# Performance work log

Measured on AMD Instinct MI355X. Metric: run time of the kernel, lower is better.

The kernel has to match this reference:

```python
import jax, jax.numpy as jnp
import numpy as np

PH, PW = 7, 7
ALPHA = 0.5


def setup_inputs() -> dict:
    key = jax.random.key(0)
    k1, k2 = jax.random.split(key)
    x = jax.random.normal(k1, (4, 128, 224, 224), dtype=jnp.float32)
    beta = jax.random.normal(k2, (1,), dtype=jnp.float32)
    return {"x": x, "beta": beta}


def reference(x, beta):
    B, C, H, W = x.shape
    Hh, Ww = H // PH, W // PW
    M = Hh * Ww
    P = PH * PW
    # non-overlapping unfold: (B,C,H,W) -> (B*M, C, P), patches row-major over (Hh,Ww),
    # pixel order within patch is row-major (i*PW+j), matching F.unfold
    flat = (
        x.reshape(B, C, Hh, PH, Ww, PW)
        .transpose(0, 2, 4, 1, 3, 5)  # (B,Hh,Ww,C,PH,PW)
        .reshape(B * M, C, P)
    )
    # channel-similarity attention: (BM,C,C)
    Sc_big = jax.nn.softmax(jnp.einsum("ncp,ndp->ncd", flat, flat), axis=-1)
    # channel covariance: (BM,C,C)
    d = flat - flat.mean(axis=-1, keepdims=True)
    cov_C = jnp.einsum("ncp,ndp->ncd", d, d) / P
    # only the top-left CxC block of L_big is ever used downstream
    # (Mc_big, cov_S and the padded S-block are dead computation in the original)
    Ec_big = jnp.einsum("ncd,ndp->ncp", Sc_big + ALPHA * cov_C, flat)  # (BM,C,P)
    # fold back (inverse of the non-overlapping unfold)
    Ec_map = (
        Ec_big.reshape(B, Hh, Ww, C, PH, PW)
        .transpose(0, 3, 1, 4, 2, 5)  # (B,C,Hh,PH,Ww,PW)
        .reshape(B, C, H, W)
    )
    attention_map = beta[0] * Ec_map + x
    out = x * attention_map
    return (out, Sc_big.reshape(B, M, C, C), cov_C.reshape(B, M, C, C), Ec_map)
```

## Files before the change

kernel.cpp:

```cpp
#include <hip/hip_runtime.h>


#define CCH 128
#define SF_STR 60
#define SA_STR 136

typedef __attribute__((ext_vector_type(8))) unsigned short ushort8v;

static __device__ __forceinline__ unsigned short f2bf(float f) {
    unsigned u = __builtin_bit_cast(unsigned, f);
    u = (u + 0x7FFFu + ((u >> 16) & 1u)) >> 16;
    return (unsigned short)u;
}
static __device__ __forceinline__ float bf2f(unsigned short h) {
    return __builtin_bit_cast(float, ((unsigned)h) << 16);
}

__global__ __launch_bounds__(512, 4)
void bdca_kernel(const float* __restrict__ x, const float* __restrict__ betap,
                 float* __restrict__ out, float* __restrict__ sc_out,
                 float* __restrict__ cov_out, float* __restrict__ ec_out)
{
    __shared__ float sF[CCH * SF_STR];
    __shared__ unsigned short sA[CCH * SA_STR];

    const int bm = blockIdx.x;
    const int b  = bm >> 10;
    const int hh = (bm >> 5) & 31;
    const int ww = bm & 31;
    const int t  = threadIdx.x;
    const float beta = betap[0];

    const float* xpatch = x + (size_t)b * (CCH * 50176) + (hh * 7) * 224 + (ww * 7);

    for (int r = t; r < CCH * 7; r += 512) {
        int c = r / 7, i = r - c * 7;
        const float* src = xpatch + (size_t)c * 50176 + i * 224;
        float* dst = &sF[c * SF_STR + i * 8];
        #pragma unroll
        for (int j = 0; j < 7; ++j) dst[j] = src[j];
    }
    __syncthreads();

    if (t < CCH) {
        const float* row = &sF[t * SF_STR];
        float s = 0.f;
        #pragma unroll
        for (int sl = 0; sl < 7; ++sl) {
            #pragma unroll
            for (int k = 0; k < 7; ++k) s += row[sl * 8 + k];
        }
        sF[t * SF_STR + 56] = s * (1.f / 49.f);
    }
    __syncthreads();

    const int rg = t >> 4;
    const int cg = t & 15;
    float g[4][8];
    #pragma unroll
    for (int i = 0; i < 4; ++i)
        #pragma unroll
        for (int j = 0; j < 8; ++j) g[i][j] = 0.f;

    #pragma unroll 1
    for (int sl = 0; sl < 7; ++sl) {
        float av[4][7];
        #pragma unroll
        for (int i = 0; i < 4; ++i) {
            const float* ap = &sF[(rg + 32 * i) * SF_STR + sl * 8];
            float4 a4 = *(const float4*)ap;
            float2 a2 = *(const float2*)(ap + 4);
            float  a6 = ap[6];
            av[i][0] = a4.x; av[i][1] = a4.y; av[i][2] = a4.z; av[i][3] = a4.w;
            av[i][4] = a2.x; av[i][5] = a2.y; av[i][6] = a6;
        }
        #pragma unroll
        for (int j = 0; j < 8; ++j) {
            const float* bp = &sF[(cg + 16 * j) * SF_STR + sl * 8];
            float4 b4 = *(const float4*)bp;
            float2 b2 = *(const float2*)(bp + 4);
            float  b6 = bp[6];
            float bv[7] = {b4.x, b4.y, b4.z, b4.w, b2.x, b2.y, b6};
            #pragma unroll
            for (int i = 0; i < 4; ++i)
                #pragma unroll
                for (int k = 0; k < 7; ++k)
                    g[i][j] = fmaf(av[i][k], bv[k], g[i][j]);
        }
    }

    const size_t scbase = (size_t)bm * (CCH * CCH);
    float mud[8];
    #pragma unroll
    for (int j = 0; j < 8; ++j) mud[j] = sF[(cg + 16 * j) * SF_STR + 56];

    #pragma unroll
    for (int i = 0; i < 4; ++i) {
        const int c = rg + 32 * i;
        float m = g[i][0];
        #pragma unroll
        for (int j = 1; j < 8; ++j) m = fmaxf(m, g[i][j]);
        #pragma unroll
        for (int msk = 1; msk <= 8; msk <<= 1) m = fmaxf(m, __shfl_xor(m, msk, 64));
        float e[8];
        float s = 0.f;
        #pragma unroll
        for (int j = 0; j < 8; ++j) { e[j] = __expf(g[i][j] - m); s += e[j]; }
        #pragma unroll
        for (int msk = 1; msk <= 8; msk <<= 1) s += __shfl_xor(s, msk, 64);
        const float rinv = 1.f / s;
        const float muc  = sF[c * SF_STR + 56];
        const size_t rowb = scbase + (size_t)c * CCH;
        #pragma unroll
        for (int j = 0; j < 8; ++j) {
            const int d = cg + 16 * j;
            const float sc = e[j] * rinv;
            const float cv = g[i][j] * (1.f / 49.f) - muc * mud[j];
            sc_out[rowb + d]  = sc;
            cov_out[rowb + d] = cv;
            sA[c * SA_STR + d] = f2bf(fmaf(0.5f, cv, sc));
        }
    }
    __syncthreads();

    if (t < 448) {
        const int dq  = t & 3;
        const int cg2 = (t >> 2) & 15;
        const int pg  = t >> 6;
        float acc[8][7];
        #pragma unroll
        for (int i = 0; i < 8; ++i)
            #pragma unroll
            for (int k = 0; k < 7; ++k) acc[i][k] = 0.f;

        #pragma unroll 1
        for (int jc = 0; jc < 4; ++jc) {
            const int d0 = dq * 32 + jc * 8;
            ushort8v av[8];
            #pragma unroll
            for (int i = 0; i < 8; ++i)
                av[i] = *(const ushort8v*)&sA[(cg2 + 16 * i) * SA_STR + d0];
            #pragma unroll
            for (int q = 0; q < 8; ++q) {
                const float* fp = &sF[(d0 + q) * SF_STR + pg * 8];
                float4 f4 = *(const float4*)fp;
                float2 f2 = *(const float2*)(fp + 4);
                float  f6 = fp[6];
                float fv[7] = {f4.x, f4.y, f4.z, f4.w, f2.x, f2.y, f6};
                #pragma unroll
                for (int i = 0; i < 8; ++i) {
                    const float aval = bf2f(av[i][q]);
                    #pragma unroll
                    for (int k = 0; k < 7; ++k)
                        acc[i][k] = fmaf(aval, fv[k], acc[i][k]);
                }
            }
        }
        #pragma unroll
        for (int i = 0; i < 8; ++i) {
            #pragma unroll
            for (int k = 0; k < 7; ++k) {
                float v = acc[i][k];
                v += __shfl_xor(v, 1, 64);
                v += __shfl_xor(v, 2, 64);
                acc[i][k] = v;
            }
        }

        #pragma unroll
        for (int i = 0; i < 8; ++i) {
            if ((i >> 1) == dq) {
                const int c = cg2 + 16 * i;
                const float* xrow = &sF[c * SF_STR + pg * 8];
                const size_t gaddr =
                    ((size_t)(b * CCH + c) * 224 + (hh * 7 + pg)) * 224 + (ww * 7);
                #pragma unroll
                for (int k = 0; k < 7; ++k) {
                    const float ec = acc[i][k];
                    const float xv = xrow[k];
                    ec_out[gaddr + k] = ec;
                    out[gaddr + k]    = xv * fmaf(beta, ec, xv);
                }
            }
        }
    }
}

extern "C" void kernel_launch(void* const* d_in, const int* in_sizes, int n_in,
                              void* d_out, int out_size, void* d_ws, size_t ws_size,
                              hipStream_t stream)
{
    const float* x    = (const float*)d_in[0];
    const float* beta = (const float*)d_in[1];
    float* out = (float*)d_out;
    float* sc  = out + 25690112;
    float* cov = sc  + 67108864;
    float* ec  = cov + 67108864;
    bdca_kernel<<<dim3(4096), dim3(512), 0, stream>>>(x, beta, out, sc, cov, ec);
}
```

Before: 1.108 ms.

## Swizzle patch smem layout, remap block order, use nontemporal stores for sc/cov

Changes the shared-memory patch buffer to a 64-float row stride with an XOR swizzle on 4-float chunks, so the vector loads in both GEMM phases avoid bank conflicts. Remaps block indices so consecutive workgroups come from different regions of the patch grid, which changes the global access pattern and L2/channel spread. Writes the large Sc and cov outputs with nontemporal stores so this streaming write traffic does not pollute the caches. The swizzle adds index arithmetic and splits each row access into two chunk addresses.

```diff
diff --git a/kernel.cpp b/kernel.cpp
--- a/kernel.cpp
+++ b/kernel.cpp
@@ -2,7 +2,7 @@
 
 
 #define CCH 128
-#define SF_STR 60
+#define SF_STR 64
 #define SA_STR 136
 
 typedef __attribute__((ext_vector_type(8))) unsigned short ushort8v;
@@ -14,6 +14,9 @@
 }
 static __device__ __forceinline__ float bf2f(unsigned short h) {
     return __builtin_bit_cast(float, ((unsigned)h) << 16);
+}
+static __device__ __forceinline__ int sfx(int row, int col) {
+    return (row << 6) + (col ^ (((row ^ (row >> 5)) & 7) << 2));
 }
 
 __global__ __launch_bounds__(512, 4)
@@ -24,7 +27,8 @@
     __shared__ float sF[CCH * SF_STR];
     __shared__ unsigned short sA[CCH * SA_STR];
 
-    const int bm = blockIdx.x;
+    const int bid = blockIdx.x;
+    const int bm  = (bid & 7) * 512 + (bid >> 3);
     const int b  = bm >> 10;
     const int hh = (bm >> 5) & 31;
     const int ww = bm & 31;
@@ -36,21 +40,22 @@
     for (int r = t; r < CCH * 7; r += 512) {
         int c = r / 7, i = r - c * 7;
         const float* src = xpatch + (size_t)c * 50176 + i * 224;
-        float* dst = &sF[c * SF_STR + i * 8];
-        #pragma unroll
-        for (int j = 0; j < 7; ++j) dst[j] = src[j];
+        float* dA = &sF[sfx(c, i * 8)];
+        float* dB = &sF[sfx(c, i * 8 + 4)];
+        dA[0] = src[0]; dA[1] = src[1]; dA[2] = src[2]; dA[3] = src[3];
+        dB[0] = src[4]; dB[1] = src[5]; dB[2] = src[6];
     }
     __syncthreads();
 
     if (t < CCH) {
-        const float* row = &sF[t * SF_STR];
         float s = 0.f;
         #pragma unroll
         for (int sl = 0; sl < 7; ++sl) {
-            #pragma unroll
-            for (int k = 0; k < 7; ++k) s += row[sl * 8 + k];
-        }
-        sF[t * SF_STR + 56] = s * (1.f / 49.f);
+            const float* pA = &sF[sfx(t, sl * 8)];
+            const float* pB = &sF[sfx(t, sl * 8 + 4)];
+            s += pA[0] + pA[1] + pA[2] + pA[3] + pB[0] + pB[1] + pB[2];
+        }
+        sF[sfx(t, 56)] = s * (1.f / 49.f);
     }
     __syncthreads();
 
@@ -67,19 +72,21 @@
         float av[4][7];
         #pragma unroll
         for (int i = 0; i < 4; ++i) {
-            const float* ap = &sF[(rg + 32 * i) * SF_STR + sl * 8];
-            float4 a4 = *(const float4*)ap;
-            float2 a2 = *(const float2*)(ap + 4);
-            float  a6 = ap[6];
+            const float* pA = &sF[sfx(rg + 32 * i, sl * 8)];
+            const float* pB = &sF[sfx(rg + 32 * i, sl * 8 + 4)];
+            float4 a4 = *(const float4*)pA;
+            float2 a2 = *(const float2*)pB;
+            float  a6 = pB[2];
             av[i][0] = a4.x; av[i][1] = a4.y; av[i][2] = a4.z; av[i][3] = a4.w;
             av[i][4] = a2.x; av[i][5] = a2.y; av[i][6] = a6;
         }
         #pragma unroll
         for (int j = 0; j < 8; ++j) {
-            const float* bp = &sF[(cg + 16 * j) * SF_STR + sl * 8];
-            float4 b4 = *(const float4*)bp;
-            float2 b2 = *(const float2*)(bp + 4);
-            float  b6 = bp[6];
+            const float* pA = &sF[sfx(cg + 16 * j, sl * 8)];
+            const float* pB = &sF[sfx(cg + 16 * j, sl * 8 + 4)];
+            float4 b4 = *(const float4*)pA;
+            float2 b2 = *(const float2*)pB;
+            float  b6 = pB[2];
             float bv[7] = {b4.x, b4.y, b4.z, b4.w, b2.x, b2.y, b6};
             #pragma unroll
             for (int i = 0; i < 4; ++i)
@@ -92,7 +99,7 @@
     const size_t scbase = (size_t)bm * (CCH * CCH);
     float mud[8];
     #pragma unroll
-    for (int j = 0; j < 8; ++j) mud[j] = sF[(cg + 16 * j) * SF_STR + 56];
+    for (int j = 0; j < 8; ++j) mud[j] = sF[sfx(cg + 16 * j, 56)];
 
     #pragma unroll
     for (int i = 0; i < 4; ++i) {
@@ -109,15 +116,15 @@
         #pragma unroll
         for (int msk = 1; msk <= 8; msk <<= 1) s += __shfl_xor(s, msk, 64);
         const float rinv = 1.f / s;
-        const float muc  = sF[c * SF_STR + 56];
+        const float muc  = sF[sfx(c, 56)];
         const size_t rowb = scbase + (size_t)c * CCH;
         #pragma unroll
         for (int j = 0; j < 8; ++j) {
             const int d = cg + 16 * j;
             const float sc = e[j] * rinv;
             const float cv = g[i][j] * (1.f / 49.f) - muc * mud[j];
-            sc_out[rowb + d]  = sc;
-            cov_out[rowb + d] = cv;
+            __builtin_nontemporal_store(sc, &sc_out[rowb + d]);
+            __builtin_nontemporal_store(cv, &cov_out[rowb + d]);
             sA[c * SA_STR + d] = f2bf(fmaf(0.5f, cv, sc));
         }
     }
@@ -142,10 +149,11 @@
                 av[i] = *(const ushort8v*)&sA[(cg2 + 16 * i) * SA_STR + d0];
             #pragma unroll
             for (int q = 0; q < 8; ++q) {
-                const float* fp = &sF[(d0 + q) * SF_STR + pg * 8];
-                float4 f4 = *(const float4*)fp;
-                float2 f2 = *(const float2*)(fp + 4);
-                float  f6 = fp[6];
+                const float* pA = &sF[sfx(d0 + q, pg * 8)];
+                const float* pB = &sF[sfx(d0 + q, pg * 8 + 4)];
+                float4 f4 = *(const float4*)pA;
+                float2 f2 = *(const float2*)pB;
+                float  f6 = pB[2];
                 float fv[7] = {f4.x, f4.y, f4.z, f4.w, f2.x, f2.y, f6};
                 #pragma unroll
                 for (int i = 0; i < 8; ++i) {
@@ -171,13 +179,14 @@
         for (int i = 0; i < 8; ++i) {
             if ((i >> 1) == dq) {
                 const int c = cg2 + 16 * i;
-                const float* xrow = &sF[c * SF_STR + pg * 8];
+                const float* xA = &sF[sfx(c, pg * 8)];
+                const float* xB = &sF[sfx(c, pg * 8 + 4)];
                 const size_t gaddr =
                     ((size_t)(b * CCH + c) * 224 + (hh * 7 + pg)) * 224 + (ww * 7);
                 #pragma unroll
                 for (int k = 0; k < 7; ++k) {
                     const float ec = acc[i][k];
-                    const float xv = xrow[k];
+                    const float xv = (k < 4) ? xA[k] : xB[k - 4];
                     ec_out[gaddr + k] = ec;
                     out[gaddr + k]    = xv * fmaf(beta, ec, xv);
                 }
```

New measurement: 1.076 ms. 2.9% less time.

## Use bf16 MFMA for Gram and output matmuls with swizzled LDS layout

Applied to the files above, without the earlier changes.

Replaces the scalar FP32 FMA loops for the channel Gram matrix and the (Sc+αcov)·flat product with MFMA 16x16x32 bf16 instructions. Patches are stored in LDS as bf16 in XOR-swizzled row-major and transposed copies, and the channel means are built with shared atomics. The change also remaps block IDs, uses nontemporal stores for the large Sc/cov outputs, and reloads x from global memory for the epilogue. In exchange, the Gram matrix that feeds softmax and covariance is now computed from bf16 inputs, which lowers accuracy. The epilogue stores are scattered, and the float4 load from src may be misaligned because ww*7 is odd.

```diff
diff --git a/kernel.cpp b/kernel.cpp
--- a/kernel.cpp
+++ b/kernel.cpp
@@ -2,18 +2,24 @@
 
 
 #define CCH 128
-#define SF_STR 60
-#define SA_STR 136
 
-typedef __attribute__((ext_vector_type(8))) unsigned short ushort8v;
+typedef __attribute__((ext_vector_type(8))) short short8v;
+typedef __attribute__((ext_vector_type(4))) float f32x4;
 
 static __device__ __forceinline__ unsigned short f2bf(float f) {
     unsigned u = __builtin_bit_cast(unsigned, f);
     u = (u + 0x7FFFu + ((u >> 16) & 1u)) >> 16;
     return (unsigned short)u;
 }
-static __device__ __forceinline__ float bf2f(unsigned short h) {
-    return __builtin_bit_cast(float, ((unsigned)h) << 16);
+
+static __device__ __forceinline__ int fbx(int c, int p) {
+    return (c << 6) + (p ^ ((c & 7) << 3));
+}
+static __device__ __forceinline__ int ftx(int p, int d) {
+    return (p << 7) + (d ^ ((p & 7) << 3));
+}
+static __device__ __forceinline__ int sax(int c, int d) {
+    return (c << 7) + (d ^ ((c & 7) << 3));
 }
 
 __global__ __launch_bounds__(512, 4)
@@ -21,165 +27,151 @@
                  float* __restrict__ out, float* __restrict__ sc_out,
                  float* __restrict__ cov_out, float* __restrict__ ec_out)
 {
-    __shared__ float sF[CCH * SF_STR];
-    __shared__ unsigned short sA[CCH * SA_STR];
+    __shared__ __align__(16) unsigned short sFB[CCH * 64];
+    __shared__ __align__(16) unsigned short sFT[64 * CCH];
+    __shared__ __align__(16) unsigned short sAm[CCH * CCH];
+    __shared__ float smu[CCH];
 
-    const int bm = blockIdx.x;
+    const int bid = blockIdx.x;
+    const int bm  = (bid & 7) * 512 + (bid >> 3);
     const int b  = bm >> 10;
     const int hh = (bm >> 5) & 31;
     const int ww = bm & 31;
     const int t  = threadIdx.x;
+    const int lane = t & 63;
+    const int w    = t >> 6;
+    const int lr   = lane & 15;
+    const int lk   = lane >> 4;
     const float beta = betap[0];
 
-    const float* xpatch = x + (size_t)b * (CCH * 50176) + (hh * 7) * 224 + (ww * 7);
-
-    for (int r = t; r < CCH * 7; r += 512) {
-        int c = r / 7, i = r - c * 7;
-        const float* src = xpatch + (size_t)c * 50176 + i * 224;
-        float* dst = &sF[c * SF_STR + i * 8];
-        #pragma unroll
-        for (int j = 0; j < 7; ++j) dst[j] = src[j];
+    {
+        short8v z = (short8v){0, 0, 0, 0, 0, 0, 0, 0};
+        short8v* pB = (short8v*)sFB;
+        short8v* pT = (short8v*)sFT;
+        pB[t] = z; pB[t + 512] = z;
+        pT[t] = z; pT[t + 512] = z;
+        if (t < CCH) smu[t] = 0.f;
     }
     __syncthreads();
 
-    if (t < CCH) {
-        const float* row = &sF[t * SF_STR];
-        float s = 0.f;
+    const float* xpatch = x + (size_t)b * (CCH * 50176) + (hh * 7) * 224 + (ww * 7);
+    for (int r = t; r < CCH * 7; r += 512) {
+        const int c = r / 7, i = r - c * 7;
+        const float* src = xpatch + (size_t)c * 50176 + i * 224;
+        float4 a4 = *(const float4*)src;
+        float2 a2 = *(const float2*)(src + 4);
+        float  a6 = src[6];
+        float v[7] = {a4.x, a4.y, a4.z, a4.w, a2.x, a2.y, a6};
+        const int p0 = i * 7;
         #pragma unroll
-        for (int sl = 0; sl < 7; ++sl) {
-            #pragma unroll
-            for (int k = 0; k < 7; ++k) s += row[sl * 8 + k];
+        for (int j = 0; j < 7; ++j) {
+            const unsigned short h = f2bf(v[j]);
+            sFB[fbx(c, p0 + j)] = h;
+            sFT[ftx(p0 + j, c)] = h;
         }
-        sF[t * SF_STR + 56] = s * (1.f / 49.f);
+        atomicAdd(&smu[c], v[0] + v[1] + v[2] + v[3] + v[4] + v[5] + v[6]);
     }
     __syncthreads();
 
-    const int rg = t >> 4;
-    const int cg = t & 15;
-    float g[4][8];
+    short8v afrag[2];
     #pragma unroll
-    for (int i = 0; i < 4; ++i)
+    for (int s = 0; s < 2; ++s)
+        afrag[s] = *(const short8v*)&sFB[fbx(16 * w + lr, s * 32 + lk * 8)];
+    f32x4 acc[8];
+    #pragma unroll
+    for (int jt = 0; jt < 8; ++jt) acc[jt] = (f32x4){0.f, 0.f, 0.f, 0.f};
+    #pragma unroll
+    for (int jt = 0; jt < 8; ++jt) {
         #pragma unroll
-        for (int j = 0; j < 8; ++j) g[i][j] = 0.f;
-
-    #pragma unroll 1
-    for (int sl = 0; sl < 7; ++sl) {
-        float av[4][7];
-        #pragma unroll
-        for (int i = 0; i < 4; ++i) {
-            const float* ap = &sF[(rg + 32 * i) * SF_STR + sl * 8];
-            float4 a4 = *(const float4*)ap;
-            float2 a2 = *(const float2*)(ap + 4);
-            float  a6 = ap[6];
-            av[i][0] = a4.x; av[i][1] = a4.y; av[i][2] = a4.z; av[i][3] = a4.w;
-            av[i][4] = a2.x; av[i][5] = a2.y; av[i][6] = a6;
-        }
-        #pragma unroll
-        for (int j = 0; j < 8; ++j) {
-            const float* bp = &sF[(cg + 16 * j) * SF_STR + sl * 8];
-            float4 b4 = *(const float4*)bp;
-            float2 b2 = *(const float2*)(bp + 4);
-            float  b6 = bp[6];
-            float bv[7] = {b4.x, b4.y, b4.z, b4.w, b2.x, b2.y, b6};
-            #pragma unroll
-            for (int i = 0; i < 4; ++i)
-                #pragma unroll
-                for (int k = 0; k < 7; ++k)
-                    g[i][j] = fmaf(av[i][k], bv[k], g[i][j]);
+        for (int s = 0; s < 2; ++s) {
+            short8v bfrag = *(const short8v*)&sFB[fbx(16 * jt + lr, s * 32 + lk * 8)];
+            acc[jt] = __builtin_amdgcn_mfma_f32_16x16x32_bf16(afrag[s], bfrag, acc[jt], 0, 0, 0);
         }
     }
 
     const size_t scbase = (size_t)bm * (CCH * CCH);
     float mud[8];
     #pragma unroll
-    for (int j = 0; j < 8; ++j) mud[j] = sF[(cg + 16 * j) * SF_STR + 56];
+    for (int jt = 0; jt < 8; ++jt) mud[jt] = smu[16 * jt + lr] * (1.f / 49.f);
 
     #pragma unroll
-    for (int i = 0; i < 4; ++i) {
-        const int c = rg + 32 * i;
-        float m = g[i][0];
+    for (int r = 0; r < 4; ++r) {
+        const int c = 16 * w + lk * 4 + r;
+        float gv[8];
         #pragma unroll
-        for (int j = 1; j < 8; ++j) m = fmaxf(m, g[i][j]);
+        for (int jt = 0; jt < 8; ++jt) gv[jt] = acc[jt][r];
+        float m = gv[0];
+        #pragma unroll
+        for (int jt = 1; jt < 8; ++jt) m = fmaxf(m, gv[jt]);
         #pragma unroll
         for (int msk = 1; msk <= 8; msk <<= 1) m = fmaxf(m, __shfl_xor(m, msk, 64));
         float e[8];
         float s = 0.f;
         #pragma unroll
-        for (int j = 0; j < 8; ++j) { e[j] = __expf(g[i][j] - m); s += e[j]; }
+        for (int jt = 0; jt < 8; ++jt) { e[jt] = __expf(gv[jt] - m); s += e[jt]; }
         #pragma unroll
         for (int msk = 1; msk <= 8; msk <<= 1) s += __shfl_xor(s, msk, 64);
         const float rinv = 1.f / s;
-        const float muc  = sF[c * SF_STR + 56];
+        const float muc  = smu[c] * (1.f / 49.f);
         const size_t rowb = scbase + (size_t)c * CCH;
         #pragma unroll
-        for (int j = 0; j < 8; ++j) {
-            const int d = cg + 16 * j;
-            const float sc = e[j] * rinv;
-            const float cv = g[i][j] * (1.f / 49.f) - muc * mud[j];
-            sc_out[rowb + d]  = sc;
-            cov_out[rowb + d] = cv;
-            sA[c * SA_STR + d] = f2bf(fmaf(0.5f, cv, sc));
+        for (int jt = 0; jt < 8; ++jt) {
+            const int d = 16 * jt + lr;
+            const float sc = e[jt] * rinv;
+            const float cv = gv[jt] * (1.f / 49.f) - muc * mud[jt];
+            __builtin_nontemporal_store(sc, &sc_out[rowb + d]);
+            __builtin_nontemporal_store(cv, &cov_out[rowb + d]);
+            sAm[sax(c, d)] = f2bf(fmaf(0.5f, cv, sc));
         }
     }
     __syncthreads();
 
-    if (t < 448) {
-        const int dq  = t & 3;
-        const int cg2 = (t >> 2) & 15;
-        const int pg  = t >> 6;
-        float acc[8][7];
+    short8v aA[4];
+    #pragma unroll
+    for (int ks = 0; ks < 4; ++ks)
+        aA[ks] = *(const short8v*)&sAm[sax(16 * w + lr, ks * 32 + lk * 8)];
+    f32x4 accE[4];
+    #pragma unroll
+    for (int nt = 0; nt < 4; ++nt) accE[nt] = (f32x4){0.f, 0.f, 0.f, 0.f};
+    #pragma unroll
+    for (int nt = 0; nt < 4; ++nt) {
         #pragma unroll
-        for (int i = 0; i < 8; ++i)
+        for (int ks = 0; ks < 4; ++ks) {
+            short8v bfr = *(const short8v*)&sFT[ftx(16 * nt + lr, ks * 32 + lk * 8)];
+            accE[nt] = __builtin_amdgcn_mfma_f32_16x16x32_bf16(aA[ks], bfr, accE[nt], 0, 0, 0);
+        }
+    }
+
+    {
+        const int cbase = 16 * w + lk * 4;
+        unsigned ga[4][4];
+        float    xv[4][4];
+        #pragma unroll
+        for (int nt = 0; nt < 4; ++nt) {
+            const int p = 16 * nt + lr;
+            const bool valid = (p < 49);
+            const int pi = p / 7;
+            const int pj = p - pi * 7;
             #pragma unroll
-            for (int k = 0; k < 7; ++k) acc[i][k] = 0.f;
-
-        #pragma unroll 1
-        for (int jc = 0; jc < 4; ++jc) {
-            const int d0 = dq * 32 + jc * 8;
-            ushort8v av[8];
-            #pragma unroll
-            for (int i = 0; i < 8; ++i)
-                av[i] = *(const ushort8v*)&sA[(cg2 + 16 * i) * SA_STR + d0];
-            #pragma unroll
-            for (int q = 0; q < 8; ++q) {
-                const float* fp = &sF[(d0 + q) * SF_STR + pg * 8];
-                float4 f4 = *(const float4*)fp;
-                float2 f2 = *(const float2*)(fp + 4);
-                float  f6 = fp[6];
-                float fv[7] = {f4.x, f4.y, f4.z, f4.w, f2.x, f2.y, f6};
-                #pragma unroll
-                for (int i = 0; i < 8; ++i) {
-                    const float aval = bf2f(av[i][q]);
-                    #pragma unroll
-                    for (int k = 0; k < 7; ++k)
-                        acc[i][k] = fmaf(aval, fv[k], acc[i][k]);
-                }
+            for (int r = 0; r < 4; ++r) {
+                const int c = cbase + r;
+                const unsigned a =
+                    ((unsigned)(b * CCH + c) * 224 + (unsigned)(hh * 7 + pi)) * 224
+                    + (unsigned)(ww * 7 + pj);
+                ga[nt][r] = a;
+                if (valid) xv[nt][r] = x[a];
             }
         }
         #pragma unroll
-        for (int i = 0; i < 8; ++i) {
-            #pragma unroll
-            for (int k = 0; k < 7; ++k) {
-                float v = acc[i][k];
-                v += __shfl_xor(v, 1, 64);
-                v += __shfl_xor(v, 2, 64);
-                acc[i][k] = v;
-            }
-        }
-
-        #pragma unroll
-        for (int i = 0; i < 8; ++i) {
-            if ((i >> 1) == dq) {
-                const int c = cg2 + 16 * i;
-                const float* xrow = &sF[c * SF_STR + pg * 8];
-                const size_t gaddr =
-                    ((size_t)(b * CCH + c) * 224 + (hh * 7 + pg)) * 224 + (ww * 7);
+        for (int nt = 0; nt < 4; ++nt) {
+            const int p = 16 * nt + lr;
+            if (p < 49) {
                 #pragma unroll
-                for (int k = 0; k < 7; ++k) {
-                    const float ec = acc[i][k];
-                    const float xv = xrow[k];
-                    ec_out[gaddr + k] = ec;
-                    out[gaddr + k]    = xv * fmaf(beta, ec, xv);
+                for (int r = 0; r < 4; ++r) {
+                    const float ec = accE[nt][r];
+                    const float v  = xv[nt][r];
+                    ec_out[ga[nt][r]] = ec;
+                    out[ga[nt][r]]    = v * fmaf(beta, ec, v);
                 }
             }
         }
```

Measured after the change: 924.8 us. -16.5%, faster.
